# Performance work log

Measured on AMD Instinct MI355X. Metric: run time of the kernel, lower is better.

Reference implementation:

```python
import jax, jax.numpy as jnp
import numpy as np

B, L, D = 4, 1024, 1024
H, DK, DV = 16, 64, 64
TEMP = float(np.power(DK, 0.5))
LN_EPS = 1e-5


def setup_inputs() -> dict:
    key = jax.random.key(0)
    ks = jax.random.split(key, 11)
    s_qk = np.sqrt(2.0 / (D + DK))
    s_v = np.sqrt(2.0 / (D + DV))
    inp = {
        'q_in': jax.random.normal(ks[0], (B, L, D), jnp.float32),
        'k_in': jax.random.normal(ks[1], (B, L, D), jnp.float32),
        'v_in': jax.random.normal(ks[2], (B, L, D), jnp.float32),
        'Wq':  jax.random.normal(ks[3], (D, H * DK), jnp.float32) * s_qk,
        'Wq2': jax.random.normal(ks[4], (D, H * DK), jnp.float32) * s_qk,
        'Wk':  jax.random.normal(ks[5], (D, H * DK), jnp.float32) * s_qk,
        'Wv':  jax.random.normal(ks[6], (D, H * DV), jnp.float32) * s_v,
        'Wo':  jax.random.normal(ks[7], (H * DV, D), jnp.float32) * np.sqrt(2.0 / (H * DV + D)),
        'ln_g': jnp.ones((D,), jnp.float32),
        'ln_b': jnp.zeros((D,), jnp.float32),
        'Er':  jax.random.normal(ks[8], (H, L, DK), jnp.float32),
        # causal mask: True above the diagonal (positions to be masked with -inf)
        'mask': jnp.triu(jnp.ones((L, L), jnp.bool_), k=1)[None].repeat(B, axis=0),
    }
    return inp


def _skew(rel):
    # rel: [H, B, Lq, Lr] with Lr == Lq. Music-Transformer skew:
    # pad one zero column on the left, reshape, drop first row.
    h, b, lq, lr = rel.shape
    rel = jnp.pad(rel, ((0, 0), (0, 0), (0, 0), (1, 0)))        # [H,B,Lq,Lr+1]
    rel = rel.reshape(h, b, lr + 1, lq)                          # [H,B,Lr+1,Lq]
    return rel[:, :, 1:, :].reshape(h, b, lq, lr)                # [H,B,Lq,Lr]


def reference(q_in, k_in, v_in, Wq, Wq2, Wk, Wv, Wo, ln_g, ln_b, Er, mask):
    residual = q_in
    # projections -> [H, B, L, d]
    def proj(x, W, d):
        return x.reshape(B * L, D).dot(W).reshape(B, L, H, d).transpose(2, 0, 1, 3)
    q = proj(q_in, Wq, DK)
    q2 = proj(q_in, Wq2, DK)
    k = proj(k_in, Wk, DK)
    v = proj(v_in, Wv, DV)

    attn = jnp.einsum('hbqd,hbkd->hbqk', q, k) / TEMP            # [H,B,Lq,Lk]
    rel = _skew(jnp.einsum('hbqd,hrd->hbqr', q2, Er)) / TEMP     # [H,B,Lq,Lk]

    m = mask[None]                                               # [1,B,Lq,Lk]
    neg = jnp.float32(-jnp.inf)
    attn = jnp.where(m, neg, attn)
    rel = jnp.where(m, neg, rel)
    p = jax.nn.softmax(attn + rel, axis=-1)                      # [H,B,Lq,Lk]

    out = jnp.einsum('hbqk,hbkd->hbqd', p, v)                    # [H,B,Lq,DV]
    out = out.transpose(1, 2, 0, 3).reshape(B, L, H * DV)
    out = out.dot(Wo)                                            # dropout is identity (eval)

    x = out + residual
    mu = x.mean(-1, keepdims=True)
    var = x.var(-1, keepdims=True)
    y = (x - mu) * jax.lax.rsqrt(var + LN_EPS) * ln_g + ln_b
    return y, p
```

## Files before the change

kernel.cpp:

```cpp
#include <hip/hip_runtime.h>

typedef __bf16 bf16;
typedef __bf16 v8bf __attribute__((ext_vector_type(8)));
typedef float v4f __attribute__((ext_vector_type(4)));

#define B_ 4
#define L_ 1024
#define D_ 1024
#define NEG (-3.0e38f)
#define MFMA16(a, b, c) __builtin_amdgcn_mfma_f32_16x16x32_bf16(a, b, c, 0, 0, 0)

__global__ __launch_bounds__(256) void wconv_kernel(
    const float* __restrict__ w0, const float* __restrict__ w1,
    const float* __restrict__ w2, const float* __restrict__ w3,
    const float* __restrict__ w4, const float* __restrict__ er,
    const float* __restrict__ qin, const float* __restrict__ kin,
    const float* __restrict__ vin,
    bf16* __restrict__ wt, bf16* __restrict__ erb,
    bf16* __restrict__ qbf, bf16* __restrict__ kbf, bf16* __restrict__ vbf)
{
    int z = blockIdx.z;
    int tx = threadIdx.x, ty = threadIdx.y;
    if (z < 5) {
        const float* src = z == 0 ? w0 : z == 1 ? w1 : z == 2 ? w2 : z == 3 ? w3 : w4;
        bf16* dst = wt + (size_t)z * 1024 * 1024;
        __shared__ float t[32][33];
        int bx = blockIdx.x * 32, by = blockIdx.y * 32;
#pragma unroll
        for (int i = 0; i < 4; i++)
            t[ty + i * 8][tx] = src[(size_t)(by + ty + i * 8) * 1024 + bx + tx];
        __syncthreads();
#pragma unroll
        for (int i = 0; i < 4; i++)
            dst[(size_t)(bx + ty + i * 8) * 1024 + by + tx] = (bf16)t[tx][ty + i * 8];
    } else if (z == 5) {
        int base = (blockIdx.y * 32 + blockIdx.x) * 256 + ty * 32 + tx;
#pragma unroll
        for (int i = 0; i < 4; i++) {
            int idx = base + i * 262144;
            erb[idx] = (bf16)er[idx];
        }
    } else {
        const float* src = z == 6 ? qin : z == 7 ? kin : vin;
        bf16* dst = z == 6 ? qbf : z == 7 ? kbf : vbf;
        int id = (blockIdx.y * 32 + blockIdx.x) * 256 + ty * 32 + tx;
#pragma unroll
        for (int i = 0; i < 4; i++) {
            int j = id * 4 + i * 1048576;
            float4 v = *(const float4*)(src + j);
            union { bf16 h[4]; uint2 u; } t;
            t.h[0] = (bf16)v.x; t.h[1] = (bf16)v.y;
            t.h[2] = (bf16)v.z; t.h[3] = (bf16)v.w;
            *(uint2*)(dst + j) = t.u;
        }
    }
}

__global__ __launch_bounds__(256) void gemm_bt(
    const bf16* __restrict__ Ab, const bf16* __restrict__ Bt,
    float* __restrict__ Cf, bf16* __restrict__ Cb,
    int M, int N, int K, int mode)
{
    __shared__ __align__(16) bf16 As[64][40];
    __shared__ __align__(16) bf16 Bs[64][40];
    int tid = threadIdx.x;
    int lane = tid & 63;
    int w = tid >> 6;
    int tm = blockIdx.y * 64, tn = blockIdx.x * 64;

    v4f acc[4];
#pragma unroll
    for (int t = 0; t < 4; t++)
#pragma unroll
        for (int i = 0; i < 4; i++) acc[t][i] = 0.f;

    int sr = tid >> 2;
    int sc = (tid & 3) * 8;
    int m15 = lane & 15;
    int kq = (lane >> 4) * 8;

    for (int k0 = 0; k0 < K; k0 += 32) {
        *(uint4*)(&As[sr][sc]) = *(const uint4*)(Ab + (size_t)(tm + sr) * K + k0 + sc);
        *(uint4*)(&Bs[sr][sc]) = *(const uint4*)(Bt + (size_t)(tn + sr) * K + k0 + sc);
        __syncthreads();

        v8bf a = *(const v8bf*)(&As[w * 16 + m15][kq]);
#pragma unroll
        for (int t = 0; t < 4; t++) {
            v8bf bfrag = *(const v8bf*)(&Bs[t * 16 + m15][kq]);
            acc[t] = MFMA16(a, bfrag, acc[t]);
        }
        __syncthreads();
    }

    int rq = lane >> 4;
#pragma unroll
    for (int t = 0; t < 4; t++) {
#pragma unroll
        for (int i = 0; i < 4; i++) {
            int row = tm + w * 16 + rq * 4 + i;
            int col = tn + t * 16 + m15;
            if (mode == 1)      Cf[(size_t)row * N + col] = acc[t][i];
            else if (mode == 0) Cb[(size_t)row * N + col] = (bf16)acc[t][i];
            else {
                int bb = row >> 10, l = row & 1023, hh = col >> 6, dv = col & 63;
                Cb[(((size_t)(bb * 16 + hh) * 64 + dv) << 10) + l] = (bf16)acc[t][i];
            }
        }
    }
}

__global__ __launch_bounds__(256) void attn_mfma(
    const bf16* __restrict__ qb, const bf16* __restrict__ q2b,
    const bf16* __restrict__ kb, const bf16* __restrict__ vt,
    const bf16* __restrict__ erb, float* __restrict__ p_out,
    bf16* __restrict__ ab)
{
    int qt = 15 - (int)blockIdx.x;
    int h = blockIdx.y, b = blockIdx.z;
    int q0 = qt << 6;
    int tid = threadIdx.x, lane = tid & 63, w = tid >> 6;
    int m15 = lane & 15, rq = lane >> 4, kq = rq * 8;
    int li0 = w * 16 + rq * 4;

    __shared__ __align__(16) bf16 Ks[64][72];
    __shared__ __align__(16) bf16 Vts[64][72];
    __shared__ __align__(16) bf16 Ers[2][64][72];
    __shared__ __align__(16) bf16 Ps[64][72];
    __shared__ __align__(16) float RELs[64][68];

    size_t pb = (size_t)(h * 4 + b) << 20;

    {
        int zr = tid >> 2, zc = (tid & 3) * 16;
        v4f zz = {0.f, 0.f, 0.f, 0.f};
        for (int kt = qt + 1; kt < 16; ++kt) {
            float* base = p_out + pb + ((size_t)(q0 + zr) << 10) + kt * 64 + zc;
#pragma unroll
            for (int i = 0; i < 4; ++i)
                __builtin_nontemporal_store(zz, (v4f*)(base + i * 4));
        }
    }

    for (int c = tid; c < 512; c += 256) {
        int r = c >> 3, col = (c & 7) * 8;
        *(uint4*)&Ks[r][col] =
            *(const uint4*)&qb[((size_t)((b << 10) + q0 + r) * 16 + h) * 64 + col];
        *(uint4*)&Vts[r][col] =
            *(const uint4*)&q2b[((size_t)((b << 10) + q0 + r) * 16 + h) * 64 + col];
    }
    __syncthreads();
    v8bf alo  = *(const v8bf*)&Ks[w * 16 + m15][kq];
    v8bf ahi  = *(const v8bf*)&Ks[w * 16 + m15][kq + 32];
    v8bf a2lo = *(const v8bf*)&Vts[w * 16 + m15][kq];
    v8bf a2hi = *(const v8bf*)&Vts[w * 16 + m15][kq + 32];

    float m_run[4], l_run[4], linv[4];
#pragma unroll
    for (int i = 0; i < 4; ++i) { m_run[i] = NEG; l_run[i] = 0.f; }
    v4f oacc[4];
#pragma unroll
    for (int t = 0; t < 4; ++t)
#pragma unroll
        for (int i = 0; i < 4; ++i) oacc[t][i] = 0.f;

    size_t kbase = ((size_t)(b << 10) * 16 + h) * 64;
    size_t vbase = ((size_t)(b * 16 + h) << 16);
    const bf16* erh = erb + ((size_t)h << 16);
    int nkt = qt + 1;

    for (int pass = 0; pass < 2; ++pass) {
        if (pass) {
#pragma unroll
            for (int i = 0; i < 4; ++i) linv[i] = 1.f / l_run[i];
        }
        for (int kt = 0; kt < nkt; ++kt) {
            int k0 = kt << 6;
            int rt0 = 15 - qt + kt;
            const bf16* erA = erh + (((size_t)rt0) << 12);
            __syncthreads();
            for (int c = tid; c < 512; c += 256) {
                int r = c >> 3, col = (c & 7) * 8;
                *(uint4*)&Ks[r][col] =
                    *(const uint4*)&kb[kbase + ((size_t)(k0 + r) << 10) + col];
                if (kt == 0)
                    *(uint4*)&Ers[rt0 & 1][r][col] =
                        *(const uint4*)&erA[((size_t)r << 6) + col];
                if (rt0 < 15)
                    *(uint4*)&Ers[~rt0 & 1][r][col] =
                        *(const uint4*)&erA[((size_t)(r + 64) << 6) + col];
                if (pass)
                    *(uint4*)&Vts[r][col] =
                        *(const uint4*)&vt[vbase + ((size_t)r << 10) + k0 + col];
            }
            __syncthreads();

            __builtin_amdgcn_s_setprio(1);
            {
                const bf16 (*EA)[72] = Ers[rt0 & 1];
#pragma unroll
                for (int ct = 0; ct < 4; ++ct) {
                    v4f acc = {0.f, 0.f, 0.f, 0.f};
                    v8bf blo = *(const v8bf*)&EA[ct * 16 + m15][kq];
                    v8bf bhi = *(const v8bf*)&EA[ct * 16 + m15][kq + 32];
                    acc = MFMA16(a2lo, blo, acc);
                    acc = MFMA16(a2hi, bhi, acc);
                    int c = ct * 16 + m15;
#pragma unroll
                    for (int i = 0; i < 4; ++i) {
                        int kl = c + li0 + i - 63;
                        if (kl >= 0) RELs[li0 + i][kl] = acc[i];
                    }
                }
            }
            if (rt0 < 15) {
                const bf16 (*EB)[72] = Ers[~rt0 & 1];
#pragma unroll
                for (int ct = 0; ct < 4; ++ct) {
                    v4f acc = {0.f, 0.f, 0.f, 0.f};
                    v8bf blo = *(const v8bf*)&EB[ct * 16 + m15][kq];
                    v8bf bhi = *(const v8bf*)&EB[ct * 16 + m15][kq + 32];
                    acc = MFMA16(a2lo, blo, acc);
                    acc = MFMA16(a2hi, bhi, acc);
                    int c = ct * 16 + m15;
#pragma unroll
                    for (int i = 0; i < 4; ++i) {
                        int kl = c + li0 + i + 1;
                        if (kl < 64) RELs[li0 + i][kl] = acc[i];
                    }
                }
            }
            v4f qk[4];
#pragma unroll
            for (int ct = 0; ct < 4; ++ct) {
                v4f acc = {0.f, 0.f, 0.f, 0.f};
                v8bf blo = *(const v8bf*)&Ks[ct * 16 + m15][kq];
                v8bf bhi = *(const v8bf*)&Ks[ct * 16 + m15][kq + 32];
                acc = MFMA16(alo, blo, acc);
                qk[ct] = MFMA16(ahi, bhi, acc);
            }
            __builtin_amdgcn_s_setprio(0);

            float sc[4][4];
#pragma unroll
            for (int ct = 0; ct < 4; ++ct)
#pragma unroll
                for (int i = 0; i < 4; ++i) {
                    int li = li0 + i;
                    int j = ct * 16 + m15;
                    float v = (qk[ct][i] + RELs[li][j]) * 0.125f;
                    sc[ct][i] = (k0 + j > q0 + li) ? NEG : v;
                }
            if (!pass) {
#pragma unroll
                for (int i = 0; i < 4; ++i) {
                    float tmax = fmaxf(fmaxf(sc[0][i], sc[1][i]), fmaxf(sc[2][i], sc[3][i]));
#pragma unroll
                    for (int off = 1; off < 16; off <<= 1)
                        tmax = fmaxf(tmax, __shfl_xor(tmax, off));
                    float mn = fmaxf(m_run[i], tmax);
                    float es = __expf(sc[0][i] - mn) + __expf(sc[1][i] - mn)
                             + __expf(sc[2][i] - mn) + __expf(sc[3][i] - mn);
#pragma unroll
                    for (int off = 1; off < 16; off <<= 1)
                        es += __shfl_xor(es, off);
                    l_run[i] = l_run[i] * __expf(m_run[i] - mn) + es;
                    m_run[i] = mn;
                }
            } else {
#pragma unroll
                for (int ct = 0; ct < 4; ++ct)
#pragma unroll
                    for (int i = 0; i < 4; ++i) {
                        int li = li0 + i;
                        int j = ct * 16 + m15;
                        float p = __expf(sc[ct][i] - m_run[i]) * linv[i];
                        __builtin_nontemporal_store(
                            p, &p_out[pb + ((size_t)(q0 + li) << 10) + k0 + j]);
                        Ps[li][j] = (bf16)p;
                    }
                v8bf plo = *(const v8bf*)&Ps[w * 16 + m15][kq];
                v8bf phi = *(const v8bf*)&Ps[w * 16 + m15][kq + 32];
                __builtin_amdgcn_s_setprio(1);
#pragma unroll
                for (int ct = 0; ct < 4; ++ct) {
                    v8bf blo = *(const v8bf*)&Vts[ct * 16 + m15][kq];
                    v8bf bhi = *(const v8bf*)&Vts[ct * 16 + m15][kq + 32];
                    oacc[ct] = MFMA16(plo, blo, oacc[ct]);
                    oacc[ct] = MFMA16(phi, bhi, oacc[ct]);
                }
                __builtin_amdgcn_s_setprio(0);
            }
        }
    }

#pragma unroll
    for (int ct = 0; ct < 4; ++ct)
#pragma unroll
        for (int i = 0; i < 4; ++i)
            ab[((size_t)((b << 10) + q0 + li0 + i) * 16 + h) * 64 + ct * 16 + m15] =
                (bf16)oacc[ct][i];
}

__global__ __launch_bounds__(256) void ln_kernel(
    const float* __restrict__ y0, const float* __restrict__ res,
    const float* __restrict__ g, const float* __restrict__ bb,
    float* __restrict__ y)
{
    int row = blockIdx.x, tid = threadIdx.x, lane = tid & 63, w = tid >> 6;
    __shared__ float rs[4], rq2[4];
    const float* xr = y0 + (size_t)row * D_;
    const float* rr = res + (size_t)row * D_;
    float x[4], sum = 0.f, sq = 0.f;
#pragma unroll
    for (int i = 0; i < 4; i++) {
        int c = tid + i * 256;
        x[i] = xr[c] + rr[c];
        sum += x[i]; sq += x[i] * x[i];
    }
#pragma unroll
    for (int off = 32; off; off >>= 1) { sum += __shfl_xor(sum, off); sq += __shfl_xor(sq, off); }
    if (lane == 0) { rs[w] = sum; rq2[w] = sq; }
    __syncthreads();
    sum = rs[0] + rs[1] + rs[2] + rs[3];
    sq  = rq2[0] + rq2[1] + rq2[2] + rq2[3];
    float mean = sum * (1.f / D_);
    float var  = sq * (1.f / D_) - mean * mean;
    float inv  = rsqrtf(var + 1e-5f);
#pragma unroll
    for (int i = 0; i < 4; i++) {
        int c = tid + i * 256;
        y[(size_t)row * D_ + c] = (x[i] - mean) * inv * g[c] + bb[c];
    }
}

extern "C" void kernel_launch(void* const* d_in, const int* in_sizes, int n_in,
                              void* d_out, int out_size, void* d_ws, size_t ws_size,
                              hipStream_t stream)
{
    const float* q_in = (const float*)d_in[0];
    const float* k_in = (const float*)d_in[1];
    const float* v_in = (const float*)d_in[2];
    const float* Wq   = (const float*)d_in[3];
    const float* Wq2  = (const float*)d_in[4];
    const float* Wk   = (const float*)d_in[5];
    const float* Wv   = (const float*)d_in[6];
    const float* Wo   = (const float*)d_in[7];
    const float* ln_g = (const float*)d_in[8];
    const float* ln_b = (const float*)d_in[9];
    const float* Er   = (const float*)d_in[10];

    float* y_out = (float*)d_out;
    float* p_out = y_out + (size_t)B_ * L_ * D_;

    char* ws = (char*)d_ws;
    const size_t MB = 1024 * 1024;
    bf16*  wT  = (bf16*)(ws);
    bf16*  erb = (bf16*)(ws + 10 * MB);
    bf16*  qb  = (bf16*)(ws + 12 * MB);
    bf16*  q2b = (bf16*)(ws + 20 * MB);
    bf16*  kb  = (bf16*)(ws + 28 * MB);
    bf16*  vtb = (bf16*)(ws + 36 * MB);
    bf16*  ab  = (bf16*)(ws + 44 * MB);
    float* y0  = (float*)(ws + 52 * MB);

    bf16* qbf = (bf16*)((char*)p_out + 160 * MB);
    bf16* kbf = (bf16*)((char*)p_out + 168 * MB);
    bf16* vbf = (bf16*)((char*)p_out + 176 * MB);

    wconv_kernel<<<dim3(32, 32, 9), dim3(32, 8), 0, stream>>>(
        Wq, Wq2, Wk, Wv, Wo, Er, q_in, k_in, v_in, wT, erb, qbf, kbf, vbf);

    gemm_bt<<<dim3(16, 64), 256, 0, stream>>>(qbf, wT + 0 * MB, nullptr, qb,  4096, 1024, 1024, 0);
    gemm_bt<<<dim3(16, 64), 256, 0, stream>>>(qbf, wT + 1 * MB, nullptr, q2b, 4096, 1024, 1024, 0);
    gemm_bt<<<dim3(16, 64), 256, 0, stream>>>(kbf, wT + 2 * MB, nullptr, kb,  4096, 1024, 1024, 0);
    gemm_bt<<<dim3(16, 64), 256, 0, stream>>>(vbf, wT + 3 * MB, nullptr, vtb, 4096, 1024, 1024, 2);

    attn_mfma<<<dim3(16, 16, 4), 256, 0, stream>>>(qb, q2b, kb, vtb, erb, p_out, ab);

    gemm_bt<<<dim3(16, 64), 256, 0, stream>>>(ab, wT + 4 * MB, y0, nullptr, 4096, 1024, 1024, 1);
    ln_kernel<<<4096, 256, 0, stream>>>(y0, q_in, ln_g, ln_b, y_out);
}
```

Baseline: 740.6 us.

## Use 128x128 direct-to-LDS GEMM, fuse Q/Q2 projections, swizzle attention LDS

Replaces the 64x64 GEMM with a 128x128 tile kernel in which each wave computes a 4x4 block of MFMA fragments and tiles are loaded with global_load_lds. The Q and Q2 projections are merged into one launch over the concatenated weights. The attention kernel moves its shared tiles to an XOR-swizzled layout, reuses the RELs buffer for P, and remaps the 1D grid so neighbouring blocks share a batch-head group. The aim is more data reuse in the GEMMs, fewer LDS bank conflicts, and fewer launches, at the cost of higher register pressure and reliance on the unpadded LDS layout being correct for the direct loads.

```diff
diff --git a/kernel.cpp b/kernel.cpp
--- a/kernel.cpp
+++ b/kernel.cpp
@@ -9,6 +9,15 @@
 #define D_ 1024
 #define NEG (-3.0e38f)
 #define MFMA16(a, b, c) __builtin_amdgcn_mfma_f32_16x16x32_bf16(a, b, c, 0, 0, 0)
+
+#define SWZ(base, r, cb) ((base) + ((r) * 128) + ((cb) ^ (((r) & 7) << 4)))
+
+typedef const __attribute__((address_space(1))) void* gas_t;
+typedef __attribute__((address_space(3))) void* las_t;
+__device__ __forceinline__ void gl_lds16(const bf16* g, bf16* l)
+{
+    __builtin_amdgcn_global_load_lds((gas_t)g, (las_t)l, 16, 0, 0);
+}
 
 __global__ __launch_bounds__(256) void wconv_kernel(
     const float* __restrict__ w0, const float* __restrict__ w1,
@@ -56,58 +65,73 @@
     }
 }
 
-__global__ __launch_bounds__(256) void gemm_bt(
+__global__ __launch_bounds__(256) void gemm128(
     const bf16* __restrict__ Ab, const bf16* __restrict__ Bt,
-    float* __restrict__ Cf, bf16* __restrict__ Cb,
-    int M, int N, int K, int mode)
-{
-    __shared__ __align__(16) bf16 As[64][40];
-    __shared__ __align__(16) bf16 Bs[64][40];
-    int tid = threadIdx.x;
-    int lane = tid & 63;
-    int w = tid >> 6;
-    int tm = blockIdx.y * 64, tn = blockIdx.x * 64;
-
-    v4f acc[4];
-#pragma unroll
-    for (int t = 0; t < 4; t++)
-#pragma unroll
-        for (int i = 0; i < 4; i++) acc[t][i] = 0.f;
-
-    int sr = tid >> 2;
-    int sc = (tid & 3) * 8;
-    int m15 = lane & 15;
-    int kq = (lane >> 4) * 8;
+    float* __restrict__ Cf, bf16* __restrict__ Cb, bf16* __restrict__ Cb2,
+    int K, int mode)
+{
+    __shared__ __align__(16) bf16 As[128 * 32];
+    __shared__ __align__(16) bf16 Bs[128 * 32];
+    int tid = threadIdx.x, lane = tid & 63, w = tid >> 6;
+    int tn = blockIdx.x * 128, tm = blockIdx.y * 128;
+    int wm = (w & 1) * 64, wn = (w >> 1) * 64;
+    int m15 = lane & 15, rq = lane >> 4, kq = rq * 8;
+
+    v4f acc[4][4];
+#pragma unroll
+    for (int m = 0; m < 4; ++m)
+#pragma unroll
+        for (int n = 0; n < 4; ++n)
+#pragma unroll
+            for (int i = 0; i < 4; ++i) acc[m][n][i] = 0.f;
+
+    int sr = lane >> 2, scb = (lane & 3) * 8;
+    const bf16* ga = Ab + (size_t)(tm + w * 32 + sr) * K + scb;
+    const bf16* gb = Bt + (size_t)(tn + w * 32 + sr) * K + scb;
+    bf16* la = As + w * 32 * 32;
+    bf16* lb = Bs + w * 32 * 32;
+    const size_t rowskip = (size_t)16 * K;
 
     for (int k0 = 0; k0 < K; k0 += 32) {
-        *(uint4*)(&As[sr][sc]) = *(const uint4*)(Ab + (size_t)(tm + sr) * K + k0 + sc);
-        *(uint4*)(&Bs[sr][sc]) = *(const uint4*)(Bt + (size_t)(tn + sr) * K + k0 + sc);
+        gl_lds16(ga + k0, la);
+        gl_lds16(ga + k0 + rowskip, la + 512);
+        gl_lds16(gb + k0, lb);
+        gl_lds16(gb + k0 + rowskip, lb + 512);
         __syncthreads();
 
-        v8bf a = *(const v8bf*)(&As[w * 16 + m15][kq]);
-#pragma unroll
-        for (int t = 0; t < 4; t++) {
-            v8bf bfrag = *(const v8bf*)(&Bs[t * 16 + m15][kq]);
-            acc[t] = MFMA16(a, bfrag, acc[t]);
-        }
+        v8bf a[4], bfr[4];
+#pragma unroll
+        for (int m = 0; m < 4; ++m)
+            a[m] = *(const v8bf*)&As[(wm + m * 16 + m15) * 32 + kq];
+#pragma unroll
+        for (int n = 0; n < 4; ++n)
+            bfr[n] = *(const v8bf*)&Bs[(wn + n * 16 + m15) * 32 + kq];
+#pragma unroll
+        for (int m = 0; m < 4; ++m)
+#pragma unroll
+            for (int n = 0; n < 4; ++n)
+                acc[m][n] = MFMA16(a[m], bfr[n], acc[m][n]);
         __syncthreads();
     }
 
-    int rq = lane >> 4;
-#pragma unroll
-    for (int t = 0; t < 4; t++) {
-#pragma unroll
-        for (int i = 0; i < 4; i++) {
-            int row = tm + w * 16 + rq * 4 + i;
-            int col = tn + t * 16 + m15;
-            if (mode == 1)      Cf[(size_t)row * N + col] = acc[t][i];
-            else if (mode == 0) Cb[(size_t)row * N + col] = (bf16)acc[t][i];
-            else {
-                int bb = row >> 10, l = row & 1023, hh = col >> 6, dv = col & 63;
-                Cb[(((size_t)(bb * 16 + hh) * 64 + dv) << 10) + l] = (bf16)acc[t][i];
-            }
-        }
-    }
+#pragma unroll
+    for (int m = 0; m < 4; ++m)
+#pragma unroll
+        for (int n = 0; n < 4; ++n)
+#pragma unroll
+            for (int i = 0; i < 4; ++i) {
+                int row = tm + wm + m * 16 + rq * 4 + i;
+                int col = tn + wn + n * 16 + m15;
+                float v = acc[m][n][i];
+                if (mode == 1)      Cf[(size_t)row * 1024 + col] = v;
+                else if (mode == 0) {
+                    bf16* dst = col < 1024 ? Cb : Cb2;
+                    dst[(size_t)row * 1024 + (col & 1023)] = (bf16)v;
+                } else {
+                    int bb = row >> 10, l = row & 1023, hh = col >> 6, dv = col & 63;
+                    Cb[(((size_t)(bb * 16 + hh) * 64 + dv) << 10) + l] = (bf16)v;
+                }
+            }
 }
 
 __global__ __launch_bounds__(256) void attn_mfma(
@@ -116,18 +140,20 @@
     const bf16* __restrict__ erb, float* __restrict__ p_out,
     bf16* __restrict__ ab)
 {
-    int qt = 15 - (int)blockIdx.x;
-    int h = blockIdx.y, b = blockIdx.z;
+    int lin = blockIdx.x;
+    int bh  = (lin & 7) | ((lin >> 7) << 3);
+    int qt  = 15 - ((lin >> 3) & 15);
+    int h = bh >> 2, b = bh & 3;
     int q0 = qt << 6;
     int tid = threadIdx.x, lane = tid & 63, w = tid >> 6;
     int m15 = lane & 15, rq = lane >> 4, kq = rq * 8;
     int li0 = w * 16 + rq * 4;
 
-    __shared__ __align__(16) bf16 Ks[64][72];
-    __shared__ __align__(16) bf16 Vts[64][72];
-    __shared__ __align__(16) bf16 Ers[2][64][72];
-    __shared__ __align__(16) bf16 Ps[64][72];
+    __shared__ __align__(16) char KsB[8192];
+    __shared__ __align__(16) char VtsB[8192];
+    __shared__ __align__(16) char ErsB[2][8192];
     __shared__ __align__(16) float RELs[64][68];
+    char* PsB = (char*)RELs;
 
     size_t pb = (size_t)(h * 4 + b) << 20;
 
@@ -143,17 +169,17 @@
     }
 
     for (int c = tid; c < 512; c += 256) {
-        int r = c >> 3, col = (c & 7) * 8;
-        *(uint4*)&Ks[r][col] =
+        int r = c >> 3, col = (c & 7) * 8, cb = (c & 7) * 16;
+        *(uint4*)SWZ(KsB, r, cb) =
             *(const uint4*)&qb[((size_t)((b << 10) + q0 + r) * 16 + h) * 64 + col];
-        *(uint4*)&Vts[r][col] =
+        *(uint4*)SWZ(VtsB, r, cb) =
             *(const uint4*)&q2b[((size_t)((b << 10) + q0 + r) * 16 + h) * 64 + col];
     }
     __syncthreads();
-    v8bf alo  = *(const v8bf*)&Ks[w * 16 + m15][kq];
-    v8bf ahi  = *(const v8bf*)&Ks[w * 16 + m15][kq + 32];
-    v8bf a2lo = *(const v8bf*)&Vts[w * 16 + m15][kq];
-    v8bf a2hi = *(const v8bf*)&Vts[w * 16 + m15][kq + 32];
+    v8bf alo  = *(const v8bf*)SWZ(KsB,  w * 16 + m15, kq * 2);
+    v8bf ahi  = *(const v8bf*)SWZ(KsB,  w * 16 + m15, kq * 2 + 64);
+    v8bf a2lo = *(const v8bf*)SWZ(VtsB, w * 16 + m15, kq * 2);
+    v8bf a2hi = *(const v8bf*)SWZ(VtsB, w * 16 + m15, kq * 2 + 64);
 
     float m_run[4], l_run[4], linv[4];
 #pragma unroll
@@ -180,29 +206,29 @@
             const bf16* erA = erh + (((size_t)rt0) << 12);
             __syncthreads();
             for (int c = tid; c < 512; c += 256) {
-                int r = c >> 3, col = (c & 7) * 8;
-                *(uint4*)&Ks[r][col] =
+                int r = c >> 3, col = (c & 7) * 8, cb = (c & 7) * 16;
+                *(uint4*)SWZ(KsB, r, cb) =
                     *(const uint4*)&kb[kbase + ((size_t)(k0 + r) << 10) + col];
                 if (kt == 0)
-                    *(uint4*)&Ers[rt0 & 1][r][col] =
+                    *(uint4*)SWZ(ErsB[rt0 & 1], r, cb) =
                         *(const uint4*)&erA[((size_t)r << 6) + col];
                 if (rt0 < 15)
-                    *(uint4*)&Ers[~rt0 & 1][r][col] =
+                    *(uint4*)SWZ(ErsB[(rt0 + 1) & 1], r, cb) =
                         *(const uint4*)&erA[((size_t)(r + 64) << 6) + col];
                 if (pass)
-                    *(uint4*)&Vts[r][col] =
+                    *(uint4*)SWZ(VtsB, r, cb) =
                         *(const uint4*)&vt[vbase + ((size_t)r << 10) + k0 + col];
             }
             __syncthreads();
 
             __builtin_amdgcn_s_setprio(1);
             {
-                const bf16 (*EA)[72] = Ers[rt0 & 1];
+                const char* EA = ErsB[rt0 & 1];
 #pragma unroll
                 for (int ct = 0; ct < 4; ++ct) {
                     v4f acc = {0.f, 0.f, 0.f, 0.f};
-                    v8bf blo = *(const v8bf*)&EA[ct * 16 + m15][kq];
-                    v8bf bhi = *(const v8bf*)&EA[ct * 16 + m15][kq + 32];
+                    v8bf blo = *(const v8bf*)SWZ(EA, ct * 16 + m15, kq * 2);
+                    v8bf bhi = *(const v8bf*)SWZ(EA, ct * 16 + m15, kq * 2 + 64);
                     acc = MFMA16(a2lo, blo, acc);
                     acc = MFMA16(a2hi, bhi, acc);
                     int c = ct * 16 + m15;
@@ -214,12 +240,12 @@
                 }
             }
             if (rt0 < 15) {
-                const bf16 (*EB)[72] = Ers[~rt0 & 1];
+                const char* EB = ErsB[(rt0 + 1) & 1];
 #pragma unroll
                 for (int ct = 0; ct < 4; ++ct) {
                     v4f acc = {0.f, 0.f, 0.f, 0.f};
-                    v8bf blo = *(const v8bf*)&EB[ct * 16 + m15][kq];
-                    v8bf bhi = *(const v8bf*)&EB[ct * 16 + m15][kq + 32];
+                    v8bf blo = *(const v8bf*)SWZ(EB, ct * 16 + m15, kq * 2);
+                    v8bf bhi = *(const v8bf*)SWZ(EB, ct * 16 + m15, kq * 2 + 64);
                     acc = MFMA16(a2lo, blo, acc);
                     acc = MFMA16(a2hi, bhi, acc);
                     int c = ct * 16 + m15;
@@ -234,8 +260,8 @@
 #pragma unroll
             for (int ct = 0; ct < 4; ++ct) {
                 v4f acc = {0.f, 0.f, 0.f, 0.f};
-                v8bf blo = *(const v8bf*)&Ks[ct * 16 + m15][kq];
-                v8bf bhi = *(const v8bf*)&Ks[ct * 16 + m15][kq + 32];
+                v8bf blo = *(const v8bf*)SWZ(KsB, ct * 16 + m15, kq * 2);
+                v8bf bhi = *(const v8bf*)SWZ(KsB, ct * 16 + m15, kq * 2 + 64);
                 acc = MFMA16(alo, blo, acc);
                 qk[ct] = MFMA16(ahi, bhi, acc);
             }
@@ -268,6 +294,7 @@
                     m_run[i] = mn;
                 }
             } else {
+                asm volatile("" ::: "memory");
 #pragma unroll
                 for (int ct = 0; ct < 4; ++ct)
 #pragma unroll
@@ -277,15 +304,16 @@
                         float p = __expf(sc[ct][i] - m_run[i]) * linv[i];
                         __builtin_nontemporal_store(
                             p, &p_out[pb + ((size_t)(q0 + li) << 10) + k0 + j]);
-                        Ps[li][j] = (bf16)p;
+                        *(bf16*)(PsB + li * 272 + j * 2) = (bf16)p;
                     }
-                v8bf plo = *(const v8bf*)&Ps[w * 16 + m15][kq];
-                v8bf phi = *(const v8bf*)&Ps[w * 16 + m15][kq + 32];
+                asm volatile("" ::: "memory");
+                v8bf plo = *(const v8bf*)(PsB + (w * 16 + m15) * 272 + kq * 2);
+                v8bf phi = *(const v8bf*)(PsB + (w * 16 + m15) * 272 + kq * 2 + 64);
                 __builtin_amdgcn_s_setprio(1);
 #pragma unroll
                 for (int ct = 0; ct < 4; ++ct) {
-                    v8bf blo = *(const v8bf*)&Vts[ct * 16 + m15][kq];
-                    v8bf bhi = *(const v8bf*)&Vts[ct * 16 + m15][kq + 32];
+                    v8bf blo = *(const v8bf*)SWZ(VtsB, ct * 16 + m15, kq * 2);
+                    v8bf bhi = *(const v8bf*)SWZ(VtsB, ct * 16 + m15, kq * 2 + 64);
                     oacc[ct] = MFMA16(plo, blo, oacc[ct]);
                     oacc[ct] = MFMA16(phi, bhi, oacc[ct]);
                 }
@@ -371,13 +399,12 @@
     wconv_kernel<<<dim3(32, 32, 9), dim3(32, 8), 0, stream>>>(
         Wq, Wq2, Wk, Wv, Wo, Er, q_in, k_in, v_in, wT, erb, qbf, kbf, vbf);
 
-    gemm_bt<<<dim3(16, 64), 256, 0, stream>>>(qbf, wT + 0 * MB, nullptr, qb,  4096, 1024, 1024, 0);
-    gemm_bt<<<dim3(16, 64), 256, 0, stream>>>(qbf, wT + 1 * MB, nullptr, q2b, 4096, 1024, 1024, 0);
-    gemm_bt<<<dim3(16, 64), 256, 0, stream>>>(kbf, wT + 2 * MB, nullptr, kb,  4096, 1024, 1024, 0);
-    gemm_bt<<<dim3(16, 64), 256, 0, stream>>>(vbf, wT + 3 * MB, nullptr, vtb, 4096, 1024, 1024, 2);
-
-    attn_mfma<<<dim3(16, 16, 4), 256, 0, stream>>>(qb, q2b, kb, vtb, erb, p_out, ab);
-
-    gemm_bt<<<dim3(16, 64), 256, 0, stream>>>(ab, wT + 4 * MB, y0, nullptr, 4096, 1024, 1024, 1);
+    gemm128<<<dim3(16, 32), 256, 0, stream>>>(qbf, wT,          nullptr, qb,  q2b,     1024, 0);
+    gemm128<<<dim3( 8, 32), 256, 0, stream>>>(kbf, wT + 2 * MB, nullptr, kb,  nullptr, 1024, 0);
+    gemm128<<<dim3( 8, 32), 256, 0, stream>>>(vbf, wT + 3 * MB, nullptr, vtb, nullptr, 1024, 2);
+
+    attn_mfma<<<dim3(1024), 256, 0, stream>>>(qb, q2b, kb, vtb, erb, p_out, ab);
+
+    gemm128<<<dim3( 8, 32), 256, 0, stream>>>(ab, wT + 4 * MB, y0, nullptr, nullptr, 1024, 1);
     ln_kernel<<<4096, 256, 0, stream>>>(y0, q_in, ln_g, ln_b, y_out);
 }
```

After: 671.5 us. 1.1x faster.
